# Kernel tuning notes

Measured on AMD Instinct MI355X. Metric: run time of the kernel, lower is better.

Reference implementation:

```python
import jax, jax.numpy as jnp
import numpy as np

N = 100000   # nodes
E = 3200000  # edges (avg degree 32)
G = 64       # graphs in batch
K = 4        # TAGConv hops
H = 16       # hidden_size
F = 2        # num_node_features
SLOPE = 0.01 # LeakyReLU default negative slope


def setup_inputs():
    key = jax.random.key(0)
    ks = jax.random.split(key, 10)
    s = 0.1
    return {
        "x": jax.random.normal(ks[0], (N, F), jnp.float32),
        "edge_index": jax.random.randint(ks[1], (2, E), 0, N),
        "edge_attr": jax.random.uniform(ks[2], (E, 7), jnp.float32),
        "batch": jnp.sort(jax.random.randint(ks[3], (N,), 0, G)),
        # conv1: K+1 hop weights [K+1, F, H] + bias [H]
        "W1": jax.random.normal(ks[4], (K + 1, F, H), jnp.float32) * s,
        "b1": jax.random.normal(ks[5], (H,), jnp.float32) * s,
        # 2 more TAGConv layers: [2, K+1, H, H] + [2, H]
        "Wl": jax.random.normal(ks[6], (2, K + 1, H, H), jnp.float32) * s,
        "bl": jax.random.normal(ks[7], (2, H), jnp.float32) * s,
        # singleLinear (reghead_layers == 1): [H, 1] + [1]
        "Ws": jax.random.normal(ks[8], (H, 1), jnp.float32) * s,
        "bs": jax.random.normal(ks[9], (1,), jnp.float32) * s,
    }


def _leaky(v):
    return jnp.where(v >= 0, v, SLOPE * v)


def _tag_conv(x, src, dst, norm, W, b):
    # out = sum_k (A_hat^k x) @ W[k] + b   (PyG TAGConv, normalize=True)
    out = x @ W[0]
    h = x
    for k in range(1, W.shape[0]):
        # gather from source, weight by normalized edge weight, scatter-add to dest
        h = jax.ops.segment_sum(h[src] * norm[:, None], dst, num_segments=x.shape[0])
        out = out + h @ W[k]
    return out + b


def reference(x, edge_index, edge_attr, batch, W1, b1, Wl, bl, Ws, bs):
    src, dst = edge_index[0], edge_index[1]
    w = edge_attr[:, 6]
    # gcn_norm without self-loops: D^{-1/2} A D^{-1/2}
    deg = jax.ops.segment_sum(w, dst, num_segments=x.shape[0])
    dinv = jnp.where(deg > 0, jax.lax.rsqrt(jnp.where(deg > 0, deg, 1.0)), 0.0)
    norm = dinv[src] * w * dinv[dst]

    h = _leaky(_tag_conv(x, src, dst, norm, W1, b1))      # dropout is eval-mode identity
    for i in range(Wl.shape[0]):
        h = _leaky(_tag_conv(h, src, dst, norm, Wl[i], bl[i]))

    # global_mean_pool over graph ids
    counts = jax.ops.segment_sum(jnp.ones((x.shape[0],), h.dtype), batch, num_segments=G)
    pooled = jax.ops.segment_sum(h, batch, num_segments=G) / jnp.maximum(counts, 1.0)[:, None]

    return pooled @ Ws + bs  # [G, 1]
```

## Files before the change

kernel.cpp:

```cpp
#include <hip/hip_runtime.h>
#include <hip/hip_fp16.h>

#define SLOPE 0.01f
#define CAP 80u

__device__ __forceinline__ float leaky(float v){ return v >= 0.f ? v : SLOPE * v; }
__device__ __forceinline__ unsigned short h2u(float f){ return __half_as_ushort(__float2half(f)); }
__device__ __forceinline__ float u2f(unsigned short u){ return __half2float(__ushort_as_half(u)); }
__device__ __forceinline__ unsigned pk2(float a, float b){
    return (unsigned)h2u(a) | ((unsigned)h2u(b) << 16);
}

__global__ __launch_bounds__(256) void k_build(const int* __restrict__ src, const int* __restrict__ dst,
                                               const float* __restrict__ attr,
                                               unsigned long long* __restrict__ packed,
                                               uint2* __restrict__ fat, int E){
    int e = blockIdx.x * 256 + threadIdx.x;
    if (e >= E) return;
    float w = attr[(size_t)e * 7 + 6];
    int d = dst[e];
    int s = src[e];
    unsigned long long add = (1ull << 40) | (unsigned long long)(w * 16777216.0f);
    unsigned long long old = atomicAdd(&packed[d], add);
    unsigned rank = (unsigned)(old >> 40);
    if (rank < CAP){
        uint2 r; r.x = (unsigned)s; r.y = __float_as_uint(w);
        fat[(size_t)d * CAP + rank] = r;
    }
}

__global__ __launch_bounds__(256) void k_dinv_bsum(const unsigned long long* __restrict__ packed,
                                                   float* __restrict__ dinv, unsigned* __restrict__ cnt,
                                                   unsigned* __restrict__ bsum, int n){
    int gid = blockIdx.x * 256 + threadIdx.x;
    unsigned c = 0;
    if (gid < n){
        unsigned long long p = packed[gid];
        float deg = (float)(p & ((1ull << 40) - 1)) * (1.0f / 16777216.0f);
        dinv[gid] = deg > 0.f ? rsqrtf(deg) : 0.f;
        c = min((unsigned)(p >> 40), CAP);
        cnt[gid] = c;
    }
    unsigned v = c;
    #pragma unroll
    for (int off = 32; off; off >>= 1) v += __shfl_down(v, off);
    __shared__ unsigned s[4];
    int lane = threadIdx.x & 63, wid = threadIdx.x >> 6;
    if (lane == 0) s[wid] = v;
    __syncthreads();
    if (threadIdx.x == 0) bsum[blockIdx.x] = s[0] + s[1] + s[2] + s[3];
}

__global__ __launch_bounds__(1024) void k_scanb(unsigned* __restrict__ bsum, unsigned* __restrict__ total_out, int nb){
    int t = threadIdx.x;
    int lane = t & 63, wid = t >> 6;
    unsigned v = t < nb ? bsum[t] : 0u;
    unsigned inc = v;
    #pragma unroll
    for (int off = 1; off < 64; off <<= 1){
        unsigned u = __shfl_up(inc, off);
        if (lane >= off) inc += u;
    }
    __shared__ unsigned sw[16];
    if (lane == 63) sw[wid] = inc;
    __syncthreads();
    if (wid == 0 && lane < 16){
        unsigned w = sw[lane];
        #pragma unroll
        for (int off = 1; off < 16; off <<= 1){
            unsigned u = __shfl_up(w, off, 16);
            if (lane >= off) w += u;
        }
        sw[lane] = w;
    }
    __syncthreads();
    unsigned waveoff = wid ? sw[wid - 1] : 0u;
    unsigned excl = waveoff + inc - v;
    if (t < nb) bsum[t] = excl;
    if (t == nb - 1) *total_out = excl + v;
}

__global__ __launch_bounds__(256) void k_scanfinal(const unsigned* __restrict__ cnt, const unsigned* __restrict__ bsum,
                                                   unsigned* __restrict__ rowptr, int n){
    int gid = blockIdx.x * 256 + threadIdx.x;
    unsigned v = gid < n ? cnt[gid] : 0u;
    int lane = threadIdx.x & 63, wid = threadIdx.x >> 6;
    unsigned inc = v;
    #pragma unroll
    for (int off = 1; off < 64; off <<= 1){
        unsigned u = __shfl_up(inc, off);
        if (lane >= off) inc += u;
    }
    __shared__ unsigned sw[4];
    if (lane == 63) sw[wid] = inc;
    __syncthreads();
    unsigned woff = 0;
    for (int i = 0; i < wid; i++) woff += sw[i];
    unsigned excl = bsum[blockIdx.x] + woff + inc - v;
    if (gid < n) rowptr[gid] = excl;
}

__global__ __launch_bounds__(256) void k_compact(const uint2* __restrict__ fat, const unsigned* __restrict__ cnt,
                                                 const unsigned* __restrict__ rowptr, const float* __restrict__ dinv,
                                                 uint2* __restrict__ csr, int n){
    int gt = blockIdx.x * 256 + threadIdx.x;
    int node = gt >> 4, k0 = gt & 15;
    if (node >= n) return;
    unsigned c = cnt[node], base = rowptr[node];
    float dv = dinv[node];
    const uint2* row = fat + (size_t)node * CAP;
    for (unsigned k = k0; k < c; k += 16){
        uint2 r = row[k];
        float nrm = dinv[r.x] * __uint_as_float(r.y) * dv;
        r.y = __float_as_uint(nrm);
        csr[base + k] = r;
    }
}

__global__ __launch_bounds__(256) void k_prop2_first(const float2* __restrict__ x, const unsigned* __restrict__ rowptr,
                                                     const uint2* __restrict__ csr,
                                                     const float* __restrict__ W1, const float* __restrict__ b1,
                                                     __half2* __restrict__ hout, __half* __restrict__ outAcc, int n){
    __shared__ float sW[64], sb[16];
    int t = threadIdx.x;
    if (t < 64) sW[t] = W1[t];
    if (t < 16) sb[t] = b1[t];
    __syncthreads();
    int gt = blockIdx.x * 256 + t;
    int node = gt >> 4, f = gt & 15;
    if (node >= n) return;
    unsigned beg = rowptr[node], end = rowptr[node + 1];
    float a0 = 0.f, a1 = 0.f;
    for (unsigned i = beg + (unsigned)f; i < end; i += 16){
        uint2 r = csr[i];
        float nrm = __uint_as_float(r.y);
        float2 h = x[r.x];
        a0 = fmaf(nrm, h.x, a0);
        a1 = fmaf(nrm, h.y, a1);
    }
    #pragma unroll
    for (int m = 1; m < 16; m <<= 1){
        a0 += __shfl_xor(a0, m, 64);
        a1 += __shfl_xor(a1, m, 64);
    }
    if (f == 0){
        __half2 hh; hh.x = __float2half(a0); hh.y = __float2half(a1);
        hout[node] = hh;
    }
    float2 xo = x[node];
    float val = sb[f] + xo.x * sW[f] + xo.y * sW[16 + f] + a0 * sW[32 + f] + a1 * sW[48 + f];
    outAcc[(size_t)node * 16 + f] = __float2half(val);
}

__global__ __launch_bounds__(256) void k_prop2_mid(const __half2* __restrict__ hin, const unsigned* __restrict__ rowptr,
                                                   const uint2* __restrict__ csr, const float* __restrict__ Wk,
                                                   __half2* __restrict__ hout, __half* __restrict__ outAcc, int n){
    __shared__ float sW[32];
    int t = threadIdx.x;
    if (t < 32) sW[t] = Wk[t];
    __syncthreads();
    int gt = blockIdx.x * 256 + t;
    int node = gt >> 4, f = gt & 15;
    if (node >= n) return;
    unsigned beg = rowptr[node], end = rowptr[node + 1];
    float a0 = 0.f, a1 = 0.f;
    for (unsigned i = beg + (unsigned)f; i < end; i += 16){
        uint2 r = csr[i];
        float nrm = __uint_as_float(r.y);
        __half2 h = hin[r.x];
        a0 = fmaf(nrm, __low2float(h), a0);
        a1 = fmaf(nrm, __high2float(h), a1);
    }
    #pragma unroll
    for (int m = 1; m < 16; m <<= 1){
        a0 += __shfl_xor(a0, m, 64);
        a1 += __shfl_xor(a1, m, 64);
    }
    if (f == 0){
        __half2 hh; hh.x = __float2half(a0); hh.y = __float2half(a1);
        hout[node] = hh;
    }
    size_t oi = (size_t)node * 16 + f;
    float val = __half2float(outAcc[oi]) + a0 * sW[f] + a1 * sW[16 + f];
    outAcc[oi] = __float2half(val);
}

__global__ __launch_bounds__(256) void k_prop2_last(const __half2* __restrict__ hin, const unsigned* __restrict__ rowptr,
                                                    const uint2* __restrict__ csr, const float* __restrict__ Wk,
                                                    const float* __restrict__ W0n, const float* __restrict__ bn,
                                                    __half* __restrict__ outAcc, __half* __restrict__ hNext, int n){
    __shared__ float sWk[32], sW0[256], sb[16];
    int t = threadIdx.x;
    if (t < 32) sWk[t] = Wk[t];
    sW0[t] = W0n[t];
    if (t < 16) sb[t] = bn[t];
    __syncthreads();
    int gt = blockIdx.x * 256 + t;
    int node = gt >> 4, f = gt & 15;
    if (node >= n) return;
    unsigned beg = rowptr[node], end = rowptr[node + 1];
    float a0 = 0.f, a1 = 0.f;
    for (unsigned i = beg + (unsigned)f; i < end; i += 16){
        uint2 r = csr[i];
        float nrm = __uint_as_float(r.y);
        __half2 h = hin[r.x];
        a0 = fmaf(nrm, __low2float(h), a0);
        a1 = fmaf(nrm, __high2float(h), a1);
    }
    #pragma unroll
    for (int m = 1; m < 16; m <<= 1){
        a0 += __shfl_xor(a0, m, 64);
        a1 += __shfl_xor(a1, m, 64);
    }
    size_t oi = (size_t)node * 16 + f;
    float val = __half2float(outAcc[oi]) + a0 * sWk[f] + a1 * sWk[16 + f];
    float hv = leaky(val);
    hNext[oi] = __float2half(hv);
    int base = (t & 63) & 48;
    float o2 = sb[f];
    #pragma unroll
    for (int fp = 0; fp < 16; fp++){
        float u = __shfl(hv, base + fp, 64);
        o2 = fmaf(u, sW0[fp * 16 + f], o2);
    }
    outAcc[oi] = __float2half(o2);
}

template<int MODE>
__global__ __launch_bounds__(256) void k_prop16(const __half* __restrict__ hin, const unsigned* __restrict__ rowptr,
                                                const uint2* __restrict__ csr, const float* __restrict__ Wk,
                                                __half* __restrict__ hout, __half* __restrict__ outAcc,
                                                __half* __restrict__ hNext,
                                                const float* __restrict__ W0n, const float* __restrict__ bn, int n){
    __shared__ float sW[256], sW2[256], sb[16];
    int t = threadIdx.x;
    sW[t] = Wk[t];
    if (MODE == 1){
        sW2[t] = W0n[t];
        if (t < 16) sb[t] = bn[t];
    }
    __syncthreads();
    int gt = blockIdx.x * 256 + t;
    int node = gt >> 2, g4 = gt & 3;
    if (node >= n) return;
    unsigned beg = rowptr[node], end = rowptr[node + 1];
    int base = (t & 63) & 60;
    int f0 = g4 * 4;
    float acc[4] = {0.f, 0.f, 0.f, 0.f};
    for (unsigned kb = beg; kb < end; kb += 4){
        unsigned idx = kb + (unsigned)g4;
        unsigned sreg = 0u; float nreg = 0.f;
        if (idx < end){
            uint2 r = csr[idx];
            sreg = r.x; nreg = __uint_as_float(r.y);
        }
        unsigned m = min(4u, end - kb);
        for (unsigned k = 0; k < m; k++){
            unsigned s = (unsigned)__shfl((int)sreg, base + (int)k, 64);
            float nm = __shfl(nreg, base + (int)k, 64);
            uint2 hv = *(const uint2*)(hin + (size_t)s * 16 + f0);
            acc[0] = fmaf(nm, u2f((unsigned short)hv.x), acc[0]);
            acc[1] = fmaf(nm, u2f((unsigned short)(hv.x >> 16)), acc[1]);
            acc[2] = fmaf(nm, u2f((unsigned short)hv.y), acc[2]);
            acc[3] = fmaf(nm, u2f((unsigned short)(hv.y >> 16)), acc[3]);
        }
    }
    if (MODE == 0){
        uint2 hw; hw.x = pk2(acc[0], acc[1]); hw.y = pk2(acc[2], acc[3]);
        *(uint2*)(hout + (size_t)node * 16 + f0) = hw;
    }
    float o[4] = {0.f, 0.f, 0.f, 0.f};
    #pragma unroll
    for (int fpg = 0; fpg < 4; fpg++){
        #pragma unroll
        for (int j = 0; j < 4; j++){
            float v = __shfl(acc[j], base + fpg, 64);
            int fp = fpg * 4 + j;
            #pragma unroll
            for (int jj = 0; jj < 4; jj++) o[jj] = fmaf(v, sW[fp * 16 + f0 + jj], o[jj]);
        }
    }
    uint2* oaP = (uint2*)(outAcc + (size_t)node * 16 + f0);
    uint2 ov = *oaP;
    float c0 = u2f((unsigned short)ov.x), c1 = u2f((unsigned short)(ov.x >> 16));
    float c2 = u2f((unsigned short)ov.y), c3 = u2f((unsigned short)(ov.y >> 16));
    if (MODE == 0){
        uint2 nv; nv.x = pk2(c0 + o[0], c1 + o[1]); nv.y = pk2(c2 + o[2], c3 + o[3]);
        *oaP = nv;
    } else {
        float hvr[4];
        hvr[0] = leaky(c0 + o[0]); hvr[1] = leaky(c1 + o[1]);
        hvr[2] = leaky(c2 + o[2]); hvr[3] = leaky(c3 + o[3]);
        uint2 hw; hw.x = pk2(hvr[0], hvr[1]); hw.y = pk2(hvr[2], hvr[3]);
        *(uint2*)(hNext + (size_t)node * 16 + f0) = hw;
        if (MODE == 1){
            float o2[4] = {sb[f0], sb[f0 + 1], sb[f0 + 2], sb[f0 + 3]};
            #pragma unroll
            for (int fpg = 0; fpg < 4; fpg++){
                #pragma unroll
                for (int j = 0; j < 4; j++){
                    float u = __shfl(hvr[j], base + fpg, 64);
                    int fp = fpg * 4 + j;
                    #pragma unroll
                    for (int jj = 0; jj < 4; jj++) o2[jj] = fmaf(u, sW2[fp * 16 + f0 + jj], o2[jj]);
                }
            }
            uint2 nv; nv.x = pk2(o2[0], o2[1]); nv.y = pk2(o2[2], o2[3]);
            *oaP = nv;
        }
    }
}

__global__ __launch_bounds__(256) void k_pool(const __half* __restrict__ h, const int* __restrict__ batch,
                                              const float* __restrict__ Ws, const float* __restrict__ bs,
                                              float* __restrict__ out, int n){
    int g = blockIdx.x;
    int lo = 0, hi = n;
    while (lo < hi){ int mid = (lo + hi) >> 1; if (batch[mid] < g) lo = mid + 1; else hi = mid; }
    int start = lo;
    lo = start; hi = n;
    while (lo < hi){ int mid = (lo + hi) >> 1; if (batch[mid] < g + 1) lo = mid + 1; else hi = mid; }
    int end = lo;
    int t = threadIdx.x;
    int slot = t >> 4, f = t & 15;
    float acc = 0.f;
    for (int node = start + slot; node < end; node += 16)
        acc += __half2float(h[(size_t)node * 16 + f]);
    __shared__ float red[256];
    red[t] = acc;
    __syncthreads();
    if (t < 16){
        float s = 0.f;
        for (int sl = 0; sl < 16; sl++) s += red[sl * 16 + t];
        float cntf = (float)max(end - start, 1);
        red[t] = (s / cntf) * Ws[t];
    }
    __syncthreads();
    if (t == 0){
        float r = bs[0];
        for (int i = 0; i < 16; i++) r += red[i];
        out[g] = r;
    }
}

extern "C" void kernel_launch(void* const* d_in, const int* in_sizes, int n_in,
                              void* d_out, int out_size, void* d_ws, size_t ws_size,
                              hipStream_t stream){
    const float* x    = (const float*)d_in[0];
    const int*   ei   = (const int*)d_in[1];
    const float* attr = (const float*)d_in[2];
    const int*   batch= (const int*)d_in[3];
    const float* W1   = (const float*)d_in[4];
    const float* b1   = (const float*)d_in[5];
    const float* Wl   = (const float*)d_in[6];
    const float* bl   = (const float*)d_in[7];
    const float* Ws   = (const float*)d_in[8];
    const float* bs   = (const float*)d_in[9];
    float* out = (float*)d_out;

    const int N = in_sizes[0] / 2;
    const int E = in_sizes[1] / 2;
    const int* src = ei;
    const int* dst = ei + E;

    char* ws = (char*)d_ws;
    size_t off = 0;
    auto alloc = [&](size_t bytes){ void* p = ws + off; off += (bytes + 255) & ~(size_t)255; return p; };
    uint2*    fat    = (uint2*)   alloc((size_t)N * CAP * 8);
    uint2*    csr    = (uint2*)   alloc((size_t)E * 8);
    unsigned long long* packed = (unsigned long long*)alloc((size_t)N * 8);
    float*    dinv   = (float*)   alloc((size_t)N * 4);
    unsigned* rowptr = (unsigned*)alloc((size_t)(N + 1) * 4);
    unsigned* cnt    = (unsigned*)alloc((size_t)N * 4);
    unsigned* bsum   = (unsigned*)alloc((size_t)1024 * 4);
    char* fr = (char*)fat;
    __half*   hA     = (__half*)  fr;                 fr += ((size_t)N * 16 * 2 + 255) & ~(size_t)255;
    __half*   hB     = (__half*)  fr;                 fr += ((size_t)N * 16 * 2 + 255) & ~(size_t)255;
    __half*   outAcc = (__half*)  fr;                 fr += ((size_t)N * 16 * 2 + 255) & ~(size_t)255;
    __half2*  h2a    = (__half2*) fr;                 fr += ((size_t)N * 4 + 255) & ~(size_t)255;
    __half2*  h2b    = (__half2*) fr;

    const int TB = 256;
    const int gE   = (E + TB - 1) / TB;
    const int gN16 = (N * 16 + TB - 1) / TB;
    const int gN4  = (N * 4 + TB - 1) / TB;
    const int nb   = (N + 255) / 256;

    hipMemsetAsync(packed, 0, (size_t)N * 8, stream);
    k_build    <<<gE, TB, 0, stream>>>(src, dst, attr, packed, fat, E);
    k_dinv_bsum<<<nb, 256, 0, stream>>>(packed, dinv, cnt, bsum, N);
    k_scanb    <<<1, 1024, 0, stream>>>(bsum, rowptr + N, nb);
    k_scanfinal<<<nb, 256, 0, stream>>>(cnt, bsum, rowptr, N);
    k_compact  <<<gN16, TB, 0, stream>>>(fat, cnt, rowptr, dinv, csr, N);

    k_prop2_first<<<gN16, TB, 0, stream>>>((const float2*)x, rowptr, csr, W1, b1, h2a, outAcc, N);
    k_prop2_mid  <<<gN16, TB, 0, stream>>>(h2a, rowptr, csr, W1 + 2 * 32, h2b, outAcc, N);
    k_prop2_mid  <<<gN16, TB, 0, stream>>>(h2b, rowptr, csr, W1 + 3 * 32, h2a, outAcc, N);
    k_prop2_last <<<gN16, TB, 0, stream>>>(h2a, rowptr, csr, W1 + 4 * 32, Wl, bl, outAcc, hA, N);

    k_prop16<0><<<gN4, TB, 0, stream>>>(hA, rowptr, csr, Wl + 1 * 256, hB, outAcc, nullptr, nullptr, nullptr, N);
    k_prop16<0><<<gN4, TB, 0, stream>>>(hB, rowptr, csr, Wl + 2 * 256, hA, outAcc, nullptr, nullptr, nullptr, N);
    k_prop16<0><<<gN4, TB, 0, stream>>>(hA, rowptr, csr, Wl + 3 * 256, hB, outAcc, nullptr, nullptr, nullptr, N);
    k_prop16<1><<<gN4, TB, 0, stream>>>(hB, rowptr, csr, Wl + 4 * 256, nullptr, outAcc, hA,
                                        Wl + 5 * 256, bl + 16, N);

    const float* W3 = Wl + 5 * 256;
    k_prop16<0><<<gN4, TB, 0, stream>>>(hA, rowptr, csr, W3 + 1 * 256, hB, outAcc, nullptr, nullptr, nullptr, N);
    k_prop16<0><<<gN4, TB, 0, stream>>>(hB, rowptr, csr, W3 + 2 * 256, hA, outAcc, nullptr, nullptr, nullptr, N);
    k_prop16<0><<<gN4, TB, 0, stream>>>(hA, rowptr, csr, W3 + 3 * 256, hB, outAcc, nullptr, nullptr, nullptr, N);
    k_prop16<2><<<gN4, TB, 0, stream>>>(hB, rowptr, csr, W3 + 4 * 256, nullptr, outAcc, hA,
                                        nullptr, nullptr, N);

    k_pool<<<64, 256, 0, stream>>>(hA, batch, Ws, bs, out, N);
}
```

Before: 639.4 us.

## Use two lanes per node with 16-byte gathers and prefetched CSR in prop16

```diff
diff --git a/kernel.cpp b/kernel.cpp
--- a/kernel.cpp
+++ b/kernel.cpp
@@ -241,71 +241,136 @@
     }
     __syncthreads();
     int gt = blockIdx.x * 256 + t;
-    int node = gt >> 2, g4 = gt & 3;
+    int node = gt >> 1, g2 = gt & 1;
     if (node >= n) return;
     unsigned beg = rowptr[node], end = rowptr[node + 1];
-    int base = (t & 63) & 60;
-    int f0 = g4 * 4;
-    float acc[4] = {0.f, 0.f, 0.f, 0.f};
-    for (unsigned kb = beg; kb < end; kb += 4){
-        unsigned idx = kb + (unsigned)g4;
-        unsigned sreg = 0u; float nreg = 0.f;
-        if (idx < end){
-            uint2 r = csr[idx];
-            sreg = r.x; nreg = __uint_as_float(r.y);
+    int base = (t & 63) & 62;
+    int f0 = g2 * 8;
+    float acc[8] = {0.f,0.f,0.f,0.f,0.f,0.f,0.f,0.f};
+    unsigned idxA = beg + (unsigned)g2;
+    unsigned idxB = idxA + 2;
+    unsigned sA = 0u, sB = 0u; float nA = 0.f, nB = 0.f;
+    if (idxA < end){ uint2 r = csr[idxA]; sA = r.x; nA = __uint_as_float(r.y); }
+    if (idxB < end){ uint2 r = csr[idxB]; sB = r.x; nB = __uint_as_float(r.y); }
+    unsigned kb = beg;
+    for (; kb + 4 <= end; kb += 4){
+        unsigned sa = sA, sbv = sB; float na = nA, nb = nB;
+        idxA += 4; idxB += 4;
+        sA = 0u; nA = 0.f; sB = 0u; nB = 0.f;
+        if (idxA < end){ uint2 r = csr[idxA]; sA = r.x; nA = __uint_as_float(r.y); }
+        if (idxB < end){ uint2 r = csr[idxB]; sB = r.x; nB = __uint_as_float(r.y); }
+        unsigned s0 = (unsigned)__shfl((int)sa,  base + 0, 64);
+        unsigned s1 = (unsigned)__shfl((int)sa,  base + 1, 64);
+        unsigned s2 = (unsigned)__shfl((int)sbv, base + 0, 64);
+        unsigned s3 = (unsigned)__shfl((int)sbv, base + 1, 64);
+        float n0 = __shfl(na, base + 0, 64);
+        float n1 = __shfl(na, base + 1, 64);
+        float n2 = __shfl(nb, base + 0, 64);
+        float n3 = __shfl(nb, base + 1, 64);
+        uint4 h0 = *(const uint4*)(hin + (size_t)s0 * 16 + f0);
+        uint4 h1 = *(const uint4*)(hin + (size_t)s1 * 16 + f0);
+        uint4 h2 = *(const uint4*)(hin + (size_t)s2 * 16 + f0);
+        uint4 h3 = *(const uint4*)(hin + (size_t)s3 * 16 + f0);
+        acc[0] = fmaf(n0, u2f((unsigned short)h0.x), acc[0]);
+        acc[1] = fmaf(n0, u2f((unsigned short)(h0.x >> 16)), acc[1]);
+        acc[2] = fmaf(n0, u2f((unsigned short)h0.y), acc[2]);
+        acc[3] = fmaf(n0, u2f((unsigned short)(h0.y >> 16)), acc[3]);
+        acc[4] = fmaf(n0, u2f((unsigned short)h0.z), acc[4]);
+        acc[5] = fmaf(n0, u2f((unsigned short)(h0.z >> 16)), acc[5]);
+        acc[6] = fmaf(n0, u2f((unsigned short)h0.w), acc[6]);
+        acc[7] = fmaf(n0, u2f((unsigned short)(h0.w >> 16)), acc[7]);
+        acc[0] = fmaf(n1, u2f((unsigned short)h1.x), acc[0]);
+        acc[1] = fmaf(n1, u2f((unsigned short)(h1.x >> 16)), acc[1]);
+        acc[2] = fmaf(n1, u2f((unsigned short)h1.y), acc[2]);
+        acc[3] = fmaf(n1, u2f((unsigned short)(h1.y >> 16)), acc[3]);
+        acc[4] = fmaf(n1, u2f((unsigned short)h1.z), acc[4]);
+        acc[5] = fmaf(n1, u2f((unsigned short)(h1.z >> 16)), acc[5]);
+        acc[6] = fmaf(n1, u2f((unsigned short)h1.w), acc[6]);
+        acc[7] = fmaf(n1, u2f((unsigned short)(h1.w >> 16)), acc[7]);
+        acc[0] = fmaf(n2, u2f((unsigned short)h2.x), acc[0]);
+        acc[1] = fmaf(n2, u2f((unsigned short)(h2.x >> 16)), acc[1]);
+        acc[2] = fmaf(n2, u2f((unsigned short)h2.y), acc[2]);
+        acc[3] = fmaf(n2, u2f((unsigned short)(h2.y >> 16)), acc[3]);
+        acc[4] = fmaf(n2, u2f((unsigned short)h2.z), acc[4]);
+        acc[5] = fmaf(n2, u2f((unsigned short)(h2.z >> 16)), acc[5]);
+        acc[6] = fmaf(n2, u2f((unsigned short)h2.w), acc[6]);
+        acc[7] = fmaf(n2, u2f((unsigned short)(h2.w >> 16)), acc[7]);
+        acc[0] = fmaf(n3, u2f((unsigned short)h3.x), acc[0]);
+        acc[1] = fmaf(n3, u2f((unsigned short)(h3.x >> 16)), acc[1]);
+        acc[2] = fmaf(n3, u2f((unsigned short)h3.y), acc[2]);
+        acc[3] = fmaf(n3, u2f((unsigned short)(h3.y >> 16)), acc[3]);
+        acc[4] = fmaf(n3, u2f((unsigned short)h3.z), acc[4]);
+        acc[5] = fmaf(n3, u2f((unsigned short)(h3.z >> 16)), acc[5]);
+        acc[6] = fmaf(n3, u2f((unsigned short)h3.w), acc[6]);
+        acc[7] = fmaf(n3, u2f((unsigned short)(h3.w >> 16)), acc[7]);
+    }
+    for (; kb < end; kb++){
+        uint2 r = csr[kb];
+        float nm = __uint_as_float(r.y);
+        uint4 hv = *(const uint4*)(hin + (size_t)r.x * 16 + f0);
+        acc[0] = fmaf(nm, u2f((unsigned short)hv.x), acc[0]);
+        acc[1] = fmaf(nm, u2f((unsigned short)(hv.x >> 16)), acc[1]);
+        acc[2] = fmaf(nm, u2f((unsigned short)hv.y), acc[2]);
+        acc[3] = fmaf(nm, u2f((unsigned short)(hv.y >> 16)), acc[3]);
+        acc[4] = fmaf(nm, u2f((unsigned short)hv.z), acc[4]);
+        acc[5] = fmaf(nm, u2f((unsigned short)(hv.z >> 16)), acc[5]);
+        acc[6] = fmaf(nm, u2f((unsigned short)hv.w), acc[6]);
+        acc[7] = fmaf(nm, u2f((unsigned short)(hv.w >> 16)), acc[7]);
+    }
+    if (MODE == 0){
+        uint4 hw;
+        hw.x = pk2(acc[0], acc[1]); hw.y = pk2(acc[2], acc[3]);
+        hw.z = pk2(acc[4], acc[5]); hw.w = pk2(acc[6], acc[7]);
+        *(uint4*)(hout + (size_t)node * 16 + f0) = hw;
+    }
+    float o[8] = {0.f,0.f,0.f,0.f,0.f,0.f,0.f,0.f};
+    #pragma unroll
+    for (int fpg = 0; fpg < 2; fpg++){
+        #pragma unroll
+        for (int j = 0; j < 8; j++){
+            float v = __shfl(acc[j], base + fpg, 64);
+            int fp = fpg * 8 + j;
+            #pragma unroll
+            for (int jj = 0; jj < 8; jj++) o[jj] = fmaf(v, sW[fp * 16 + f0 + jj], o[jj]);
         }
-        unsigned m = min(4u, end - kb);
-        for (unsigned k = 0; k < m; k++){
-            unsigned s = (unsigned)__shfl((int)sreg, base + (int)k, 64);
-            float nm = __shfl(nreg, base + (int)k, 64);
-            uint2 hv = *(const uint2*)(hin + (size_t)s * 16 + f0);
-            acc[0] = fmaf(nm, u2f((unsigned short)hv.x), acc[0]);
-            acc[1] = fmaf(nm, u2f((unsigned short)(hv.x >> 16)), acc[1]);
-            acc[2] = fmaf(nm, u2f((unsigned short)hv.y), acc[2]);
-            acc[3] = fmaf(nm, u2f((unsigned short)(hv.y >> 16)), acc[3]);
-        }
-    }
+    }
+    uint4* oaP = (uint4*)(outAcc + (size_t)node * 16 + f0);
+    uint4 ov = *oaP;
+    float c[8];
+    c[0] = u2f((unsigned short)ov.x); c[1] = u2f((unsigned short)(ov.x >> 16));
+    c[2] = u2f((unsigned short)ov.y); c[3] = u2f((unsigned short)(ov.y >> 16));
+    c[4] = u2f((unsigned short)ov.z); c[5] = u2f((unsigned short)(ov.z >> 16));
+    c[6] = u2f((unsigned short)ov.w); c[7] = u2f((unsigned short)(ov.w >> 16));
     if (MODE == 0){
-        uint2 hw; hw.x = pk2(acc[0], acc[1]); hw.y = pk2(acc[2], acc[3]);
-        *(uint2*)(hout + (size_t)node * 16 + f0) = hw;
-    }
-    float o[4] = {0.f, 0.f, 0.f, 0.f};
-    #pragma unroll
-    for (int fpg = 0; fpg < 4; fpg++){
-        #pragma unroll
-        for (int j = 0; j < 4; j++){
-            float v = __shfl(acc[j], base + fpg, 64);
-            int fp = fpg * 4 + j;
-            #pragma unroll
-            for (int jj = 0; jj < 4; jj++) o[jj] = fmaf(v, sW[fp * 16 + f0 + jj], o[jj]);
-        }
-    }
-    uint2* oaP = (uint2*)(outAcc + (size_t)node * 16 + f0);
-    uint2 ov = *oaP;
-    float c0 = u2f((unsigned short)ov.x), c1 = u2f((unsigned short)(ov.x >> 16));
-    float c2 = u2f((unsigned short)ov.y), c3 = u2f((unsigned short)(ov.y >> 16));
-    if (MODE == 0){
-        uint2 nv; nv.x = pk2(c0 + o[0], c1 + o[1]); nv.y = pk2(c2 + o[2], c3 + o[3]);
+        uint4 nv;
+        nv.x = pk2(c[0] + o[0], c[1] + o[1]); nv.y = pk2(c[2] + o[2], c[3] + o[3]);
+        nv.z = pk2(c[4] + o[4], c[5] + o[5]); nv.w = pk2(c[6] + o[6], c[7] + o[7]);
         *oaP = nv;
     } else {
-        float hvr[4];
-        hvr[0] = leaky(c0 + o[0]); hvr[1] = leaky(c1 + o[1]);
-        hvr[2] = leaky(c2 + o[2]); hvr[3] = leaky(c3 + o[3]);
-        uint2 hw; hw.x = pk2(hvr[0], hvr[1]); hw.y = pk2(hvr[2], hvr[3]);
-        *(uint2*)(hNext + (size_t)node * 16 + f0) = hw;
+        float hvr[8];
+        #pragma unroll
+        for (int j = 0; j < 8; j++) hvr[j] = leaky(c[j] + o[j]);
+        uint4 hw;
+        hw.x = pk2(hvr[0], hvr[1]); hw.y = pk2(hvr[2], hvr[3]);
+        hw.z = pk2(hvr[4], hvr[5]); hw.w = pk2(hvr[6], hvr[7]);
+        *(uint4*)(hNext + (size_t)node * 16 + f0) = hw;
         if (MODE == 1){
-            float o2[4] = {sb[f0], sb[f0 + 1], sb[f0 + 2], sb[f0 + 3]};
+            float o2[8];
             #pragma unroll
-            for (int fpg = 0; fpg < 4; fpg++){
+            for (int jj = 0; jj < 8; jj++) o2[jj] = sb[f0 + jj];
+            #pragma unroll
+            for (int fpg = 0; fpg < 2; fpg++){
                 #pragma unroll
-                for (int j = 0; j < 4; j++){
+                for (int j = 0; j < 8; j++){
                     float u = __shfl(hvr[j], base + fpg, 64);
-                    int fp = fpg * 4 + j;
+                    int fp = fpg * 8 + j;
                     #pragma unroll
-                    for (int jj = 0; jj < 4; jj++) o2[jj] = fmaf(u, sW2[fp * 16 + f0 + jj], o2[jj]);
+                    for (int jj = 0; jj < 8; jj++) o2[jj] = fmaf(u, sW2[fp * 16 + f0 + jj], o2[jj]);
                 }
             }
-            uint2 nv; nv.x = pk2(o2[0], o2[1]); nv.y = pk2(o2[2], o2[3]);
+            uint4 nv;
+            nv.x = pk2(o2[0], o2[1]); nv.y = pk2(o2[2], o2[3]);
+            nv.z = pk2(o2[4], o2[5]); nv.w = pk2(o2[6], o2[7]);
             *oaP = nv;
         }
     }
@@ -383,7 +448,7 @@
     const int TB = 256;
     const int gE   = (E + TB - 1) / TB;
     const int gN16 = (N * 16 + TB - 1) / TB;
-    const int gN4  = (N * 4 + TB - 1) / TB;
+    const int gN2  = (N * 2 + TB - 1) / TB;
     const int nb   = (N + 255) / 256;
 
     hipMemsetAsync(packed, 0, (size_t)N * 8, stream);
@@ -398,17 +463,17 @@
     k_prop2_mid  <<<gN16, TB, 0, stream>>>(h2b, rowptr, csr, W1 + 3 * 32, h2a, outAcc, N);
     k_prop2_last <<<gN16, TB, 0, stream>>>(h2a, rowptr, csr, W1 + 4 * 32, Wl, bl, outAcc, hA, N);
 
-    k_prop16<0><<<gN4, TB, 0, stream>>>(hA, rowptr, csr, Wl + 1 * 256, hB, outAcc, nullptr, nullptr, nullptr, N);
-    k_prop16<0><<<gN4, TB, 0, stream>>>(hB, rowptr, csr, Wl + 2 * 256, hA, outAcc, nullptr, nullptr, nullptr, N);
-    k_prop16<0><<<gN4, TB, 0, stream>>>(hA, rowptr, csr, Wl + 3 * 256, hB, outAcc, nullptr, nullptr, nullptr, N);
-    k_prop16<1><<<gN4, TB, 0, stream>>>(hB, rowptr, csr, Wl + 4 * 256, nullptr, outAcc, hA,
+    k_prop16<0><<<gN2, TB, 0, stream>>>(hA, rowptr, csr, Wl + 1 * 256, hB, outAcc, nullptr, nullptr, nullptr, N);
+    k_prop16<0><<<gN2, TB, 0, stream>>>(hB, rowptr, csr, Wl + 2 * 256, hA, outAcc, nullptr, nullptr, nullptr, N);
+    k_prop16<0><<<gN2, TB, 0, stream>>>(hA, rowptr, csr, Wl + 3 * 256, hB, outAcc, nullptr, nullptr, nullptr, N);
+    k_prop16<1><<<gN2, TB, 0, stream>>>(hB, rowptr, csr, Wl + 4 * 256, nullptr, outAcc, hA,
                                         Wl + 5 * 256, bl + 16, N);
 
     const float* W3 = Wl + 5 * 256;
-    k_prop16<0><<<gN4, TB, 0, stream>>>(hA, rowptr, csr, W3 + 1 * 256, hB, outAcc, nullptr, nullptr, nullptr, N);
-    k_prop16<0><<<gN4, TB, 0, stream>>>(hB, rowptr, csr, W3 + 2 * 256, hA, outAcc, nullptr, nullptr, nullptr, N);
-    k_prop16<0><<<gN4, TB, 0, stream>>>(hA, rowptr, csr, W3 + 3 * 256, hB, outAcc, nullptr, nullptr, nullptr, N);
-    k_prop16<2><<<gN4, TB, 0, stream>>>(hB, rowptr, csr, W3 + 4 * 256, nullptr, outAcc, hA,
+    k_prop16<0><<<gN2, TB, 0, stream>>>(hA, rowptr, csr, W3 + 1 * 256, hB, outAcc, nullptr, nullptr, nullptr, N);
+    k_prop16<0><<<gN2, TB, 0, stream>>>(hB, rowptr, csr, W3 + 2 * 256, hA, outAcc, nullptr, nullptr, nullptr, N);
+    k_prop16<0><<<gN2, TB, 0, stream>>>(hA, rowptr, csr, W3 + 3 * 256, hB, outAcc, nullptr, nullptr, nullptr, N);
+    k_prop16<2><<<gN2, TB, 0, stream>>>(hB, rowptr, csr, W3 + 4 * 256, nullptr, outAcc, hA,
                                         nullptr, nullptr, N);
 
     k_pool<<<64, 256, 0, stream>>>(hA, batch, Ws, bs, out, N);
```

New measurement: 647.9 us. About the same (+1.3%).
